# Kernel optimization log

Hardware: AMD Instinct MI355X
Metric: run time of the kernel (lower is better)

The kernel has to match this reference:

```python
import jax, jax.numpy as jnp
import numpy as np

N = 50000
E = 800000
NFEAT, NHID, NCODE, NCLASS = 512, 256, 64, 40


def setup_inputs() -> dict:
    key = jax.random.key(0)
    ks = jax.random.split(key, 16)
    def glorot(k, shape):
        lim = 1.0 / np.sqrt(shape[0])
        return jax.random.uniform(k, shape, jnp.float32, -lim, lim)
    return {
        "x": jax.random.normal(ks[0], (N, NFEAT), jnp.float32),
        "edge_src": jax.random.randint(ks[1], (E,), 0, N, jnp.int32),
        "edge_dst": jax.random.randint(ks[2], (E,), 0, N, jnp.int32),
        "edge_weight": jax.random.uniform(ks[3], (E,), jnp.float32),
        "eps": jax.random.normal(ks[4], (N, NCODE), jnp.float32),
        # gc1: GraphConvolution(nfeat, nhid)
        "W1": glorot(ks[5], (NFEAT, NHID)),
        "b1": glorot(ks[6], (NHID,)),
        # fc11 / fc12: Linear(nhid, ncode)
        "W_mu": glorot(ks[7], (NHID, NCODE)),
        "b_mu": glorot(ks[8], (NCODE,)),
        "W_lv": glorot(ks[9], (NHID, NCODE)),
        "b_lv": glorot(ks[10], (NCODE,)),
        # fc2: Linear(ncode, nhid)
        "W_dec": glorot(ks[11], (NCODE, NHID)),
        "b_dec": glorot(ks[12], (NHID,)),
        # gc2: GraphConvolution(2*nhid, nclass)
        "W2": glorot(ks[13], (2 * NHID, NCLASS)),
        "b2": glorot(ks[14], (NCLASS,)),
    }


def spmm(edge_src, edge_dst, edge_weight, support):
    # spmm(adj, support): gather rows at src, scale by edge weight, scatter-add to dst
    msgs = support[edge_src] * edge_weight[:, None]  # [E, d]
    return jax.ops.segment_sum(msgs, edge_dst, num_segments=N)


def reference(x, edge_src, edge_dst, edge_weight, eps,
              W1, b1, W_mu, b_mu, W_lv, b_lv, W_dec, b_dec, W2, b2):
    # gc1: relu(spmm(adj, x @ W1) + b1)
    h1 = jax.nn.relu(spmm(edge_src, edge_dst, edge_weight, x @ W1) + b1)
    # dropout is identity in inference mode
    mu = h1 @ W_mu + b_mu
    log_var = h1 @ W_lv + b_lv
    # reparametrize: std = exp(log_var) (as in source, no 0.5 factor)
    z = mu + eps * jnp.exp(log_var)
    # decode
    x1 = jax.nn.relu(z @ W_dec + b_dec)
    x1 = jnp.concatenate([x1, h1], axis=1)  # [N, 2*nhid]
    # gc2
    logits = spmm(edge_src, edge_dst, edge_weight, x1 @ W2) + b2
    return jax.nn.log_softmax(logits, axis=1)
```

## Files before the change

### kernel.cpp

```cpp
#include <hip/hip_runtime.h>
#include <math.h>

#define N_NODES 50000
#define N_EDGES 800000
#define NFEAT 512
#define NHID 256
#define NCODE 64
#define NCLASS 40
#define NCLS_PAD 48
#define NB_SCAN 196

typedef __attribute__((ext_vector_type(8))) short short8;
typedef __attribute__((ext_vector_type(8))) unsigned short ushort8;
typedef __attribute__((ext_vector_type(4))) unsigned short ushort4v;
typedef __attribute__((ext_vector_type(4))) float floatx4;

__device__ inline unsigned short f2bf(float f) {
    unsigned u = __builtin_bit_cast(unsigned, f);
    u += 0x7fff + ((u >> 16) & 1);
    return (unsigned short)(u >> 16);
}
__device__ inline float bf2f(unsigned short h) {
    return __builtin_bit_cast(float, (unsigned)h << 16);
}
__device__ inline unsigned pkbf(float lo, float hi) {
    unsigned r;
    asm("v_cvt_pk_bf16_f32 %0, %1, %2" : "=v"(r) : "v"(lo), "v"(hi));
    return r;
}
__device__ inline void gload_lds16(const void* g, void* l) {
    __builtin_amdgcn_global_load_lds(
        (const __attribute__((address_space(1))) unsigned int*)g,
        (__attribute__((address_space(3))) unsigned int*)l, 16, 0, 0);
}

__global__ __launch_bounds__(256) void hist_kernel(const int* __restrict__ dst,
                                                   int* __restrict__ counts) {
    int t = blockIdx.x * 256 + threadIdx.x;
    if (t < N_EDGES) atomicAdd(&counts[dst[t]], 1);
}

__global__ __launch_bounds__(256) void scan_block_sums(const int* __restrict__ counts,
                                                       int* __restrict__ blockSums) {
    __shared__ int red[256];
    int t = threadIdx.x;
    int i = blockIdx.x * 256 + t;
    red[t] = (i < N_NODES) ? counts[i] : 0;
    __syncthreads();
#pragma unroll
    for (int off = 128; off > 0; off >>= 1) {
        if (t < off) red[t] += red[t + off];
        __syncthreads();
    }
    if (t == 0) blockSums[blockIdx.x] = red[0];
}

__global__ __launch_bounds__(256) void scan_block_offsets(const int* __restrict__ blockSums,
                                                          int* __restrict__ blockOffsets,
                                                          int* __restrict__ offsets) {
    __shared__ int s[256];
    int t = threadIdx.x;
    int v = (t < NB_SCAN) ? blockSums[t] : 0;
    s[t] = v;
    __syncthreads();
#pragma unroll
    for (int off = 1; off < 256; off <<= 1) {
        int x = (t >= off) ? s[t - off] : 0;
        __syncthreads();
        s[t] += x;
        __syncthreads();
    }
    if (t < NB_SCAN) blockOffsets[t] = s[t] - v;
    if (t == 255) offsets[N_NODES] = s[255];
}

__global__ __launch_bounds__(256) void scan_final(const int* __restrict__ counts,
                                                  const int* __restrict__ blockOffsets,
                                                  int* __restrict__ offsets) {
    __shared__ int s[256];
    int t = threadIdx.x;
    int i = blockIdx.x * 256 + t;
    int v = (i < N_NODES) ? counts[i] : 0;
    s[t] = v;
    __syncthreads();
#pragma unroll
    for (int off = 1; off < 256; off <<= 1) {
        int x = (t >= off) ? s[t - off] : 0;
        __syncthreads();
        s[t] += x;
        __syncthreads();
    }
    if (i < N_NODES) offsets[i] = blockOffsets[blockIdx.x] + s[t] - v;
}

__global__ __launch_bounds__(256) void scatter_kernel(const int* __restrict__ dst,
                                                      const int* __restrict__ src,
                                                      const float* __restrict__ w,
                                                      const int* __restrict__ offsets,
                                                      int* __restrict__ cursor,
                                                      int2* __restrict__ edges) {
    int t = blockIdx.x * 256 + threadIdx.x;
    if (t < N_EDGES) {
        int d = dst[t];
        int pos = offsets[d] + atomicAdd(&cursor[d], 1);
        edges[pos] = make_int2(src[t], __builtin_bit_cast(int, w[t]));
    }
}

__global__ __launch_bounds__(256) void wprep_kernel(const float* __restrict__ W1,
                                                    const float* __restrict__ W2,
                                                    const float* __restrict__ W_mu,
                                                    const float* __restrict__ W_lv,
                                                    const float* __restrict__ W_dec,
                                                    unsigned short* __restrict__ W1t,
                                                    unsigned short* __restrict__ W2bt,
                                                    unsigned short* __restrict__ W_mulvt,
                                                    unsigned short* __restrict__ W_dect) {
    int idx = blockIdx.x * 256 + threadIdx.x;
    if (idx < NFEAT * NHID) {
        int k = idx >> 8;
        int n = idx & 255;
        W1t[(size_t)n * NFEAT + k] = f2bf(W1[idx]);
    } else if (idx < NFEAT * NHID + NCLS_PAD * NFEAT) {
        int i2 = idx - NFEAT * NHID;
        int n = i2 >> 9;
        int k = i2 & 511;
        W2bt[i2] = (n < NCLASS) ? f2bf(W2[(size_t)k * NCLASS + n]) : (unsigned short)0;
    } else if (idx < NFEAT * NHID + NCLS_PAD * NFEAT + 128 * 256) {
        int i2 = idx - NFEAT * NHID - NCLS_PAD * NFEAT;
        int j = i2 >> 8;
        int k = i2 & 255;
        float v = (j < 64) ? W_mu[(size_t)k * NCODE + j] : W_lv[(size_t)k * NCODE + (j - 64)];
        W_mulvt[i2] = f2bf(v);
    } else if (idx < NFEAT * NHID + NCLS_PAD * NFEAT + 128 * 256 + 256 * 64) {
        int i2 = idx - NFEAT * NHID - NCLS_PAD * NFEAT - 128 * 256;
        int n = i2 >> 6;
        int k = i2 & 63;
        W_dect[i2] = f2bf(W_dec[(size_t)k * NHID + n]);
    }
}

__global__ __launch_bounds__(256) void gemm1_mfma(const float* __restrict__ A,
                                                  const unsigned short* __restrict__ Bt,
                                                  unsigned short* __restrict__ C) {
    __shared__ unsigned short As[128 * 64];
    __shared__ unsigned short Bs[128 * 64];
    int t = threadIdx.x;
    int wave = t >> 6, lane = t & 63;
    int quad = lane >> 4, m16 = lane & 15;
    int wr = wave >> 1, wc = wave & 1;
    int m0 = blockIdx.x * 128;
    int n0 = blockIdx.y * 128;

    int srow = t >> 3;
    int kcs = (t & 7) ^ (srow & 7);
    const float* Ap[4];
#pragma unroll
    for (int r = 0; r < 4; ++r) {
        int ga = m0 + r * 32 + srow;
        if (ga >= N_NODES) ga = N_NODES - 1;
        Ap[r] = A + (size_t)ga * NFEAT + kcs * 8;
    }
    const unsigned short* Bbase = Bt + (size_t)(n0 + srow) * NFEAT + kcs * 8;

    floatx4 acc[4][4];
#pragma unroll
    for (int m = 0; m < 4; ++m)
#pragma unroll
        for (int n = 0; n < 4; ++n) acc[m][n] = (floatx4){0.f, 0.f, 0.f, 0.f};

    float4 a0[4], a1[4];
#pragma unroll
    for (int r = 0; r < 4; ++r) {
        a0[r] = *(const float4*)(Ap[r]);
        a1[r] = *(const float4*)(Ap[r] + 4);
    }

#pragma unroll
    for (int k0 = 0; k0 < NFEAT; k0 += 64) {
        uint4 aw[4];
#pragma unroll
        for (int r = 0; r < 4; ++r) {
            aw[r].x = pkbf(a0[r].x, a0[r].y);
            aw[r].y = pkbf(a0[r].z, a0[r].w);
            aw[r].z = pkbf(a1[r].x, a1[r].y);
            aw[r].w = pkbf(a1[r].z, a1[r].w);
        }
        __syncthreads();
#pragma unroll
        for (int r = 0; r < 4; ++r)
            gload_lds16(Bbase + (size_t)r * 32 * NFEAT + k0, &Bs[(r * 256 + wave * 64) * 8]);
#pragma unroll
        for (int r = 0; r < 4; ++r) *(uint4*)&As[(r * 256 + t) * 8] = aw[r];
        __syncthreads();
        if (k0 + 64 < NFEAT) {
#pragma unroll
            for (int r = 0; r < 4; ++r) {
                a0[r] = *(const float4*)(Ap[r] + k0 + 64);
                a1[r] = *(const float4*)(Ap[r] + k0 + 68);
            }
        }
#pragma unroll
        for (int c = 0; c < 2; ++c) {
            int sw = ((c * 4 + quad) ^ (m16 & 7)) * 8;
            short8 af[4], bfr[4];
#pragma unroll
            for (int m = 0; m < 4; ++m)
                af[m] = *(const short8*)&As[(wr * 64 + m * 16 + m16) * 64 + sw];
#pragma unroll
            for (int n = 0; n < 4; ++n)
                bfr[n] = *(const short8*)&Bs[(wc * 64 + n * 16 + m16) * 64 + sw];
#pragma unroll
            for (int m = 0; m < 4; ++m)
#pragma unroll
                for (int n = 0; n < 4; ++n)
                    acc[m][n] =
                        __builtin_amdgcn_mfma_f32_16x16x32_bf16(af[m], bfr[n], acc[m][n], 0, 0, 0);
        }
    }
#pragma unroll
    for (int m = 0; m < 4; ++m) {
#pragma unroll
        for (int n = 0; n < 4; ++n) {
            int col = n0 + wc * 64 + n * 16 + m16;
#pragma unroll
            for (int r = 0; r < 4; ++r) {
                int row = m0 + wr * 64 + m * 16 + quad * 4 + r;
                if (row < N_NODES) C[(size_t)row * NHID + col] = f2bf(acc[m][n][r]);
            }
        }
    }
}

__global__ __launch_bounds__(256) void spmm1_kernel(const int* __restrict__ offsets,
                                                    const int2* __restrict__ edges,
                                                    const unsigned short* __restrict__ S1b,
                                                    const float* __restrict__ b1,
                                                    unsigned short* __restrict__ x1cat) {
    int n = blockIdx.x * 4 + (threadIdx.x >> 6);
    int lane = threadIdx.x & 63;
    int beg = offsets[n], end = offsets[n + 1];
    float ax = 0.f, ay = 0.f, az = 0.f, aw = 0.f;
    int i = beg;
    for (; i + 8 <= end; i += 8) {
        int2 e[8];
        ushort4v r[8];
#pragma unroll
        for (int u = 0; u < 8; u++) e[u] = edges[i + u];
#pragma unroll
        for (int u = 0; u < 8; u++)
            r[u] = *(const ushort4v*)&S1b[(size_t)e[u].x * NHID + lane * 4];
#pragma unroll
        for (int u = 0; u < 8; u++) {
            float ww = __builtin_bit_cast(float, e[u].y);
            ax += ww * bf2f(r[u][0]);
            ay += ww * bf2f(r[u][1]);
            az += ww * bf2f(r[u][2]);
            aw += ww * bf2f(r[u][3]);
        }
    }
    for (; i < end; i++) {
        int2 e = edges[i];
        float ww = __builtin_bit_cast(float, e.y);
        ushort4v r = *(const ushort4v*)&S1b[(size_t)e.x * NHID + lane * 4];
        ax += ww * bf2f(r[0]); ay += ww * bf2f(r[1]);
        az += ww * bf2f(r[2]); aw += ww * bf2f(r[3]);
    }
    float4 bb = *(const float4*)&b1[lane * 4];
    ushort4v hb;
    hb[0] = f2bf(fmaxf(ax + bb.x, 0.f));
    hb[1] = f2bf(fmaxf(ay + bb.y, 0.f));
    hb[2] = f2bf(fmaxf(az + bb.z, 0.f));
    hb[3] = f2bf(fmaxf(aw + bb.w, 0.f));
    *(ushort4v*)&x1cat[(size_t)n * (2 * NHID) + NHID + lane * 4] = hb;
}

__global__ __launch_bounds__(256) void mulv_mfma(const unsigned short* __restrict__ x1cat,
                                                 const unsigned short* __restrict__ W_mulvt,
                                                 const float* __restrict__ b_mu,
                                                 const float* __restrict__ b_lv,
                                                 unsigned short* __restrict__ mulv) {
    __shared__ unsigned short Bs[64][264];
    int t = threadIdx.x;
    int wave = t >> 6, lane = t & 63;
    int quad = lane >> 4, m16 = lane & 15;
    int m0 = blockIdx.x * 64;
    int ybase = blockIdx.y * 64;

#pragma unroll
    for (int r = 0; r < 8; ++r) {
        int c = r * 256 + t;
        int row = c >> 5, col = (c & 31) * 8;
        *(ushort8*)&Bs[row][col] = *(const ushort8*)&W_mulvt[(size_t)(ybase + row) * 256 + col];
    }
    int arow = m0 + wave * 16 + m16;
    if (arow >= N_NODES) arow = N_NODES - 1;
    const unsigned short* Abase = x1cat + (size_t)arow * 512 + 256 + quad * 8;

    floatx4 acc[4];
#pragma unroll
    for (int i = 0; i < 4; ++i) acc[i] = (floatx4){0.f, 0.f, 0.f, 0.f};
    __syncthreads();

#pragma unroll
    for (int k0 = 0; k0 < 256; k0 += 32) {
        short8 af = *(const short8*)(Abase + k0);
#pragma unroll
        for (int nt = 0; nt < 4; ++nt) {
            short8 bfr = *(const short8*)&Bs[nt * 16 + m16][k0 + quad * 8];
            acc[nt] = __builtin_amdgcn_mfma_f32_16x16x32_bf16(af, bfr, acc[nt], 0, 0, 0);
        }
    }
    const float* bias_v = blockIdx.y ? b_lv : b_mu;
#pragma unroll
    for (int nt = 0; nt < 4; ++nt) {
        int j = nt * 16 + m16;
        float bias = bias_v[j];
#pragma unroll
        for (int r = 0; r < 4; ++r) {
            int row = m0 + wave * 16 + quad * 4 + r;
            if (row < N_NODES) mulv[(size_t)row * 128 + ybase + j] = f2bf(acc[nt][r] + bias);
        }
    }
}

__global__ __launch_bounds__(256) void zdec_mfma(const unsigned short* __restrict__ mulv,
                                                 const float* __restrict__ eps,
                                                 const unsigned short* __restrict__ W_dect,
                                                 const float* __restrict__ b_dec,
                                                 unsigned short* __restrict__ x1cat) {
    __shared__ unsigned short Bs[256][72];
    int t = threadIdx.x;
    int wave = t >> 6, lane = t & 63;
    int quad = lane >> 4, m16 = lane & 15;
    int m0 = blockIdx.x * 64;

#pragma unroll
    for (int r = 0; r < 8; ++r) {
        int c = r * 256 + t;
        int row = c >> 3, col = (c & 7) * 8;
        *(ushort8*)&Bs[row][col] = *(const ushort8*)&W_dect[(size_t)row * 64 + col];
    }
    int grow = m0 + wave * 16 + m16;
    if (grow >= N_NODES) grow = N_NODES - 1;

    floatx4 acc[16];
#pragma unroll
    for (int i = 0; i < 16; ++i) acc[i] = (floatx4){0.f, 0.f, 0.f, 0.f};
    __syncthreads();

#pragma unroll
    for (int ks = 0; ks < 2; ++ks) {
        int c0 = ks * 32 + quad * 8;
        ushort8 mu8 = *(const ushort8*)&mulv[(size_t)grow * 128 + c0];
        ushort8 lv8 = *(const ushort8*)&mulv[(size_t)grow * 128 + 64 + c0];
        float4 e0 = *(const float4*)&eps[(size_t)grow * 64 + c0];
        float4 e1 = *(const float4*)&eps[(size_t)grow * 64 + c0 + 4];
        ushort8 zz;
        zz[0] = f2bf(bf2f(mu8[0]) + e0.x * expf(bf2f(lv8[0])));
        zz[1] = f2bf(bf2f(mu8[1]) + e0.y * expf(bf2f(lv8[1])));
        zz[2] = f2bf(bf2f(mu8[2]) + e0.z * expf(bf2f(lv8[2])));
        zz[3] = f2bf(bf2f(mu8[3]) + e0.w * expf(bf2f(lv8[3])));
        zz[4] = f2bf(bf2f(mu8[4]) + e1.x * expf(bf2f(lv8[4])));
        zz[5] = f2bf(bf2f(mu8[5]) + e1.y * expf(bf2f(lv8[5])));
        zz[6] = f2bf(bf2f(mu8[6]) + e1.z * expf(bf2f(lv8[6])));
        zz[7] = f2bf(bf2f(mu8[7]) + e1.w * expf(bf2f(lv8[7])));
        short8 af = *(short8*)&zz;
#pragma unroll
        for (int nt = 0; nt < 16; ++nt) {
            short8 bfr = *(const short8*)&Bs[nt * 16 + m16][ks * 32 + quad * 8];
            acc[nt] = __builtin_amdgcn_mfma_f32_16x16x32_bf16(af, bfr, acc[nt], 0, 0, 0);
        }
    }
#pragma unroll
    for (int nt = 0; nt < 16; ++nt) {
        int col = nt * 16 + m16;
        float bias = b_dec[col];
#pragma unroll
        for (int r = 0; r < 4; ++r) {
            int row = m0 + wave * 16 + quad * 4 + r;
            if (row < N_NODES)
                x1cat[(size_t)row * 512 + col] = f2bf(fmaxf(acc[nt][r] + bias, 0.f));
        }
    }
}

__global__ __launch_bounds__(256) void gemm2_mfma(const unsigned short* __restrict__ Xb,
                                                  const unsigned short* __restrict__ Bt,
                                                  unsigned short* __restrict__ S2b) {
    __shared__ unsigned short Bs[NCLS_PAD][520];
    int t = threadIdx.x;
    int wave = t >> 6, lane = t & 63;
    int quad = lane >> 4, m16 = lane & 15;
    int m0 = blockIdx.x * 64;

#pragma unroll
    for (int r = 0; r < 12; ++r) {
        int cidx = r * 256 + t;
        int row = cidx >> 6, col = (cidx & 63) * 8;
        *(ushort8*)&Bs[row][col] = *(const ushort8*)&Bt[(size_t)row * NFEAT + col];
    }

    int arow = m0 + wave * 16 + m16;
    if (arow >= N_NODES) arow = N_NODES - 1;
    const unsigned short* Abase = Xb + (size_t)arow * NFEAT + quad * 8;

    floatx4 acc[3];
#pragma unroll
    for (int i = 0; i < 3; i++) acc[i] = (floatx4){0.f, 0.f, 0.f, 0.f};
    __syncthreads();

#pragma unroll
    for (int k0 = 0; k0 < NFEAT; k0 += 32) {
        short8 af = *(const short8*)(Abase + k0);
#pragma unroll
        for (int nt = 0; nt < 3; nt++) {
            short8 bfr = *(const short8*)&Bs[nt * 16 + m16][k0 + quad * 8];
            acc[nt] = __builtin_amdgcn_mfma_f32_16x16x32_bf16(af, bfr, acc[nt], 0, 0, 0);
        }
    }
#pragma unroll
    for (int nt = 0; nt < 3; nt++) {
        int col = nt * 16 + m16;
#pragma unroll
        for (int r = 0; r < 4; r++) {
            int row = m0 + wave * 16 + quad * 4 + r;
            if (row < N_NODES) S2b[(size_t)row * 64 + col] = f2bf(acc[nt][r]);
        }
    }
#pragma unroll
    for (int r = 0; r < 4; r++) {
        int row = m0 + wave * 16 + quad * 4 + r;
        if (row < N_NODES) S2b[(size_t)row * 64 + 48 + m16] = 0;
    }
}

__global__ __launch_bounds__(256) void spmm2_softmax_kernel(const int* __restrict__ offsets,
                                                            const int2* __restrict__ edges,
                                                            const unsigned short* __restrict__ S2b,
                                                            const float* __restrict__ b2,
                                                            float* __restrict__ out) {
    int wave = threadIdx.x >> 6;
    int lane = threadIdx.x & 63;
    int g = lane >> 3, c = lane & 7;
    int n = blockIdx.x * 4 + wave;
    int beg = offsets[n], end = offsets[n + 1];
    float acc[8];
#pragma unroll
    for (int j = 0; j < 8; ++j) acc[j] = 0.f;

    int i = beg;
    for (; i + 16 <= end; i += 16) {
        int2 e0 = edges[i + g];
        int2 e1 = edges[i + 8 + g];
        ushort8 r0 = *(const ushort8*)&S2b[(size_t)e0.x * 64 + c * 8];
        ushort8 r1 = *(const ushort8*)&S2b[(size_t)e1.x * 64 + c * 8];
        float w0 = __builtin_bit_cast(float, e0.y);
        float w1 = __builtin_bit_cast(float, e1.y);
#pragma unroll
        for (int j = 0; j < 8; ++j) acc[j] += w0 * bf2f(r0[j]) + w1 * bf2f(r1[j]);
    }
    for (; i < end; i += 8) {
        int idx = i + g;
        int ic = (idx < end) ? idx : (end - 1);
        int2 e = edges[ic];
        float ww = (idx < end) ? __builtin_bit_cast(float, e.y) : 0.f;
        ushort8 r = *(const ushort8*)&S2b[(size_t)e.x * 64 + c * 8];
#pragma unroll
        for (int j = 0; j < 8; ++j) acc[j] += ww * bf2f(r[j]);
    }
#pragma unroll
    for (int off = 8; off <= 32; off <<= 1) {
#pragma unroll
        for (int j = 0; j < 8; ++j) acc[j] += __shfl_xor(acc[j], off);
    }
    float v[8];
#pragma unroll
    for (int j = 0; j < 8; ++j) {
        int col = c * 8 + j;
        v[j] = (col < NCLASS) ? (acc[j] + b2[col]) : -INFINITY;
    }
    float m = v[0];
#pragma unroll
    for (int j = 1; j < 8; ++j) m = fmaxf(m, v[j]);
#pragma unroll
    for (int off = 1; off <= 4; off <<= 1) m = fmaxf(m, __shfl_xor(m, off));
    float ssum = 0.f;
    float ex[8];
#pragma unroll
    for (int j = 0; j < 8; ++j) {
        ex[j] = (v[j] > -INFINITY) ? expf(v[j] - m) : 0.f;
        ssum += ex[j];
    }
#pragma unroll
    for (int off = 1; off <= 4; off <<= 1) ssum += __shfl_xor(ssum, off);
    float lse = logf(ssum);
    if (g == 0) {
#pragma unroll
        for (int j = 0; j < 8; ++j) {
            int col = c * 8 + j;
            if (col < NCLASS) out[(size_t)n * NCLASS + col] = v[j] - m - lse;
        }
    }
}

extern "C" void kernel_launch(void* const* d_in, const int* in_sizes, int n_in,
                              void* d_out, int out_size, void* d_ws, size_t ws_size,
                              hipStream_t stream) {
    const float* x     = (const float*)d_in[0];
    const int*   esrc  = (const int*)d_in[1];
    const int*   edst  = (const int*)d_in[2];
    const float* ew    = (const float*)d_in[3];
    const float* eps   = (const float*)d_in[4];
    const float* W1    = (const float*)d_in[5];
    const float* b1    = (const float*)d_in[6];
    const float* W_mu  = (const float*)d_in[7];
    const float* b_mu  = (const float*)d_in[8];
    const float* W_lv  = (const float*)d_in[9];
    const float* b_lv  = (const float*)d_in[10];
    const float* W_dec = (const float*)d_in[11];
    const float* b_dec = (const float*)d_in[12];
    const float* W2    = (const float*)d_in[13];
    const float* b2    = (const float*)d_in[14];
    float* out = (float*)d_out;

    unsigned short* support1b = (unsigned short*)d_ws;
    unsigned short* x1cat = support1b + (size_t)N_NODES * NHID;
    unsigned short* S2b = x1cat + (size_t)N_NODES * 2 * NHID;
    unsigned short* W1t    = S2b + (size_t)N_NODES * 64;
    unsigned short* W2bt   = W1t + (size_t)NHID * NFEAT;
    unsigned short* W_mulvt = W2bt + (size_t)NCLS_PAD * NFEAT;
    unsigned short* W_dect  = W_mulvt + 128 * 256;
    unsigned short* mulv    = W_dect + 256 * 64;
    int*   counts   = (int*)(((size_t)(mulv + (size_t)N_NODES * 128) + 3) & ~(size_t)3);
    int*   cursor   = counts + N_NODES;
    int*   offsets  = cursor + N_NODES;
    int*   blockSums    = offsets + N_NODES + 1;
    int*   blockOffsets = blockSums + NB_SCAN;
    int2*  edges    = (int2*)(blockOffsets + NB_SCAN);
    edges = (int2*)(((size_t)edges + 7) & ~(size_t)7);
    size_t need = (size_t)((char*)(edges + N_EDGES) - (char*)d_ws);
    if (ws_size < need) return;

    hipMemsetAsync(counts, 0, 2 * N_NODES * sizeof(int), stream);
    hist_kernel<<<(N_EDGES + 255) / 256, 256, 0, stream>>>(edst, counts);
    scan_block_sums<<<NB_SCAN, 256, 0, stream>>>(counts, blockSums);
    scan_block_offsets<<<1, 256, 0, stream>>>(blockSums, blockOffsets, offsets);
    scan_final<<<NB_SCAN, 256, 0, stream>>>(counts, blockOffsets, offsets);
    scatter_kernel<<<(N_EDGES + 255) / 256, 256, 0, stream>>>(edst, esrc, ew, offsets, cursor,
                                                              edges);

    wprep_kernel<<<800, 256, 0, stream>>>(W1, W2, W_mu, W_lv, W_dec, W1t, W2bt, W_mulvt, W_dect);
    dim3 g1((N_NODES + 127) / 128, 2);
    gemm1_mfma<<<g1, 256, 0, stream>>>(x, W1t, support1b);
    spmm1_kernel<<<N_NODES / 4, 256, 0, stream>>>(offsets, edges, support1b, b1, x1cat);
    dim3 gm((N_NODES + 63) / 64, 2);
    mulv_mfma<<<gm, 256, 0, stream>>>(x1cat, W_mulvt, b_mu, b_lv, mulv);
    zdec_mfma<<<(N_NODES + 63) / 64, 256, 0, stream>>>(mulv, eps, W_dect, b_dec, x1cat);
    gemm2_mfma<<<(N_NODES + 63) / 64, 256, 0, stream>>>(x1cat, W2bt, S2b);
    spmm2_softmax_kernel<<<N_NODES / 4, 256, 0, stream>>>(offsets, edges, S2b, b2, out);
}
```

Baseline: 438.8 us.

## Fuse mu/logvar GEMM, reparametrization and decoder GEMM into one kernel

Merges the mulv and zdec kernels into a single kernel. Each block keeps its h1 tile in registers, computes mu and log_var in sequence using a shared LDS buffer, forms z in LDS, and then runs the decoder GEMM. This removes the mulv round trip to global memory, one kernel launch, and the second read of h1 that the two-column-block split caused. The cost is a larger LDS footprint, more barriers and serialized phases within each block, and the same x1cat buffer is both read and written under restrict qualifiers, touching disjoint column halves.

```diff
diff --git a/kernel.cpp b/kernel.cpp
--- a/kernel.cpp
+++ b/kernel.cpp
@@ -275,100 +275,93 @@
     *(ushort4v*)&x1cat[(size_t)n * (2 * NHID) + NHID + lane * 4] = hb;
 }
 
-__global__ __launch_bounds__(256) void mulv_mfma(const unsigned short* __restrict__ x1cat,
-                                                 const unsigned short* __restrict__ W_mulvt,
+__global__ __launch_bounds__(256) void mlp_fused(const unsigned short* __restrict__ x1cat_ro,
+                                                 const float* __restrict__ eps,
                                                  const float* __restrict__ b_mu,
                                                  const float* __restrict__ b_lv,
-                                                 unsigned short* __restrict__ mulv) {
-    __shared__ unsigned short Bs[64][264];
+                                                 const unsigned short* __restrict__ W_mulvt,
+                                                 const float* __restrict__ b_dec,
+                                                 const unsigned short* __restrict__ W_dect,
+                                                 unsigned short* __restrict__ x1cat) {
+    __shared__ unsigned short buf[23040];
     int t = threadIdx.x;
     int wave = t >> 6, lane = t & 63;
     int quad = lane >> 4, m16 = lane & 15;
     int m0 = blockIdx.x * 64;
-    int ybase = blockIdx.y * 64;
+
+    int arow = m0 + wave * 16 + m16;
+    if (arow >= N_NODES) arow = N_NODES - 1;
+    short8 hfr[8];
+#pragma unroll
+    for (int k = 0; k < 8; ++k)
+        hfr[k] = *(const short8*)(x1cat_ro + (size_t)arow * 512 + 256 + k * 32 + quad * 8);
 
 #pragma unroll
     for (int r = 0; r < 8; ++r) {
         int c = r * 256 + t;
         int row = c >> 5, col = (c & 31) * 8;
-        *(ushort8*)&Bs[row][col] = *(const ushort8*)&W_mulvt[(size_t)(ybase + row) * 256 + col];
-    }
-    int arow = m0 + wave * 16 + m16;
-    if (arow >= N_NODES) arow = N_NODES - 1;
-    const unsigned short* Abase = x1cat + (size_t)arow * 512 + 256 + quad * 8;
-
-    floatx4 acc[4];
-#pragma unroll
-    for (int i = 0; i < 4; ++i) acc[i] = (floatx4){0.f, 0.f, 0.f, 0.f};
-    __syncthreads();
-
-#pragma unroll
-    for (int k0 = 0; k0 < 256; k0 += 32) {
-        short8 af = *(const short8*)(Abase + k0);
+        *(ushort8*)&buf[row * 264 + col] = *(const ushort8*)&W_mulvt[(size_t)row * 256 + col];
+    }
+    floatx4 amu[4], alv[4];
+#pragma unroll
+    for (int i = 0; i < 4; ++i) amu[i] = (floatx4){0.f, 0.f, 0.f, 0.f};
+    __syncthreads();
+#pragma unroll
+    for (int k = 0; k < 8; ++k) {
 #pragma unroll
         for (int nt = 0; nt < 4; ++nt) {
-            short8 bfr = *(const short8*)&Bs[nt * 16 + m16][k0 + quad * 8];
-            acc[nt] = __builtin_amdgcn_mfma_f32_16x16x32_bf16(af, bfr, acc[nt], 0, 0, 0);
-        }
-    }
-    const float* bias_v = blockIdx.y ? b_lv : b_mu;
-#pragma unroll
-    for (int nt = 0; nt < 4; ++nt) {
-        int j = nt * 16 + m16;
-        float bias = bias_v[j];
+            short8 bfr = *(const short8*)&buf[(nt * 16 + m16) * 264 + k * 32 + quad * 8];
+            amu[nt] = __builtin_amdgcn_mfma_f32_16x16x32_bf16(hfr[k], bfr, amu[nt], 0, 0, 0);
+        }
+    }
+    __syncthreads();
+#pragma unroll
+    for (int r = 0; r < 8; ++r) {
+        int c = r * 256 + t;
+        int row = c >> 5, col = (c & 31) * 8;
+        *(ushort8*)&buf[row * 264 + col] =
+            *(const ushort8*)&W_mulvt[(size_t)(64 + row) * 256 + col];
+    }
+#pragma unroll
+    for (int i = 0; i < 4; ++i) alv[i] = (floatx4){0.f, 0.f, 0.f, 0.f};
+    __syncthreads();
+#pragma unroll
+    for (int k = 0; k < 8; ++k) {
+#pragma unroll
+        for (int nt = 0; nt < 4; ++nt) {
+            short8 bfr = *(const short8*)&buf[(nt * 16 + m16) * 264 + k * 32 + quad * 8];
+            alv[nt] = __builtin_amdgcn_mfma_f32_16x16x32_bf16(hfr[k], bfr, alv[nt], 0, 0, 0);
+        }
+    }
+    __syncthreads();
+#pragma unroll
+    for (int q = 0; q < 4; ++q) {
+        int col = q * 16 + m16;
+        float bmu = b_mu[col], blv = b_lv[col];
 #pragma unroll
         for (int r = 0; r < 4; ++r) {
             int row = m0 + wave * 16 + quad * 4 + r;
-            if (row < N_NODES) mulv[(size_t)row * 128 + ybase + j] = f2bf(acc[nt][r] + bias);
-        }
-    }
-}
-
-__global__ __launch_bounds__(256) void zdec_mfma(const unsigned short* __restrict__ mulv,
-                                                 const float* __restrict__ eps,
-                                                 const unsigned short* __restrict__ W_dect,
-                                                 const float* __restrict__ b_dec,
-                                                 unsigned short* __restrict__ x1cat) {
-    __shared__ unsigned short Bs[256][72];
-    int t = threadIdx.x;
-    int wave = t >> 6, lane = t & 63;
-    int quad = lane >> 4, m16 = lane & 15;
-    int m0 = blockIdx.x * 64;
-
+            int er = (row < N_NODES) ? row : N_NODES - 1;
+            float z = (amu[q][r] + bmu) + eps[(size_t)er * NCODE + col] * expf(alv[q][r] + blv);
+            buf[(wave * 16 + quad * 4 + r) * 72 + col] = f2bf(z);
+        }
+    }
 #pragma unroll
     for (int r = 0; r < 8; ++r) {
         int c = r * 256 + t;
         int row = c >> 3, col = (c & 7) * 8;
-        *(ushort8*)&Bs[row][col] = *(const ushort8*)&W_dect[(size_t)row * 64 + col];
-    }
-    int grow = m0 + wave * 16 + m16;
-    if (grow >= N_NODES) grow = N_NODES - 1;
-
+        *(ushort8*)&buf[4608 + row * 72 + col] = *(const ushort8*)&W_dect[(size_t)row * 64 + col];
+    }
+    __syncthreads();
     floatx4 acc[16];
 #pragma unroll
     for (int i = 0; i < 16; ++i) acc[i] = (floatx4){0.f, 0.f, 0.f, 0.f};
-    __syncthreads();
-
 #pragma unroll
     for (int ks = 0; ks < 2; ++ks) {
-        int c0 = ks * 32 + quad * 8;
-        ushort8 mu8 = *(const ushort8*)&mulv[(size_t)grow * 128 + c0];
-        ushort8 lv8 = *(const ushort8*)&mulv[(size_t)grow * 128 + 64 + c0];
-        float4 e0 = *(const float4*)&eps[(size_t)grow * 64 + c0];
-        float4 e1 = *(const float4*)&eps[(size_t)grow * 64 + c0 + 4];
-        ushort8 zz;
-        zz[0] = f2bf(bf2f(mu8[0]) + e0.x * expf(bf2f(lv8[0])));
-        zz[1] = f2bf(bf2f(mu8[1]) + e0.y * expf(bf2f(lv8[1])));
-        zz[2] = f2bf(bf2f(mu8[2]) + e0.z * expf(bf2f(lv8[2])));
-        zz[3] = f2bf(bf2f(mu8[3]) + e0.w * expf(bf2f(lv8[3])));
-        zz[4] = f2bf(bf2f(mu8[4]) + e1.x * expf(bf2f(lv8[4])));
-        zz[5] = f2bf(bf2f(mu8[5]) + e1.y * expf(bf2f(lv8[5])));
-        zz[6] = f2bf(bf2f(mu8[6]) + e1.z * expf(bf2f(lv8[6])));
-        zz[7] = f2bf(bf2f(mu8[7]) + e1.w * expf(bf2f(lv8[7])));
-        short8 af = *(short8*)&zz;
+        short8 af = *(const short8*)&buf[(wave * 16 + m16) * 72 + ks * 32 + quad * 8];
 #pragma unroll
         for (int nt = 0; nt < 16; ++nt) {
-            short8 bfr = *(const short8*)&Bs[nt * 16 + m16][ks * 32 + quad * 8];
+            short8 bfr = *(const short8*)&buf[4608 + (nt * 16 + m16) * 72 + ks * 32 + quad * 8];
             acc[nt] = __builtin_amdgcn_mfma_f32_16x16x32_bf16(af, bfr, acc[nt], 0, 0, 0);
         }
     }
@@ -531,8 +524,7 @@
     unsigned short* W2bt   = W1t + (size_t)NHID * NFEAT;
     unsigned short* W_mulvt = W2bt + (size_t)NCLS_PAD * NFEAT;
     unsigned short* W_dect  = W_mulvt + 128 * 256;
-    unsigned short* mulv    = W_dect + 256 * 64;
-    int*   counts   = (int*)(((size_t)(mulv + (size_t)N_NODES * 128) + 3) & ~(size_t)3);
+    int*   counts   = (int*)(((size_t)(W_dect + 256 * 64) + 3) & ~(size_t)3);
     int*   cursor   = counts + N_NODES;
     int*   offsets  = cursor + N_NODES;
     int*   blockSums    = offsets + N_NODES + 1;
@@ -554,9 +546,8 @@
     dim3 g1((N_NODES + 127) / 128, 2);
     gemm1_mfma<<<g1, 256, 0, stream>>>(x, W1t, support1b);
     spmm1_kernel<<<N_NODES / 4, 256, 0, stream>>>(offsets, edges, support1b, b1, x1cat);
-    dim3 gm((N_NODES + 63) / 64, 2);
-    mulv_mfma<<<gm, 256, 0, stream>>>(x1cat, W_mulvt, b_mu, b_lv, mulv);
-    zdec_mfma<<<(N_NODES + 63) / 64, 256, 0, stream>>>(mulv, eps, W_dect, b_dec, x1cat);
+    mlp_fused<<<(N_NODES + 63) / 64, 256, 0, stream>>>(x1cat, eps, b_mu, b_lv, W_mulvt, b_dec,
+                                                       W_dect, x1cat);
     gemm2_mfma<<<(N_NODES + 63) / 64, 256, 0, stream>>>(x1cat, W2bt, S2b);
     spmm2_softmax_kernel<<<N_NODES / 4, 256, 0, stream>>>(offsets, edges, S2b, b2, out);
 }
```

Result: no change. 437.4 us (-0.3%).
